# Performance work log

Measured on AMD Instinct MI355X. Metric: run time of the kernel, lower is better.

The kernel has to match this reference:

```python
import jax, jax.numpy as jnp
import numpy as np

B, T, H, HV, K, V = 8, 4096, 4, 8, 128, 128
SOFTPLUS_BETA = 1.0
SOFTPLUS_THRESHOLD = 20.0
USE_QK_L2NORM = True


def setup_inputs() -> dict:
    key = jax.random.key(0)
    ks = jax.random.split(key, 9)
    return {
        "A_log": jax.random.normal(ks[0], (HV,), jnp.float32) * 0.1,
        "a": jax.random.normal(ks[1], (B, T, HV), jnp.float32),
        "dt_bias": jax.random.normal(ks[2], (HV,), jnp.float32),
        "q": jax.random.normal(ks[3], (B, T, H, K), jnp.float32),
        "k": jax.random.normal(ks[4], (B, T, H, K), jnp.float32),
        "v": jax.random.normal(ks[5], (B, T, HV, V), jnp.float32),
        "b": jax.random.normal(ks[6], (B, T, HV), jnp.float32),
        "initial_state_source": jax.random.normal(ks[7], (B, HV, K, V), jnp.float32),
        "initial_state_indices": jax.random.randint(ks[8], (B,), 0, B, jnp.int32),
    }


def _softplus(x):
    # matches kernel: where(beta*x <= thr, log(1+exp(beta*x))/beta, x)
    bx = SOFTPLUS_BETA * x
    safe = jnp.minimum(bx, SOFTPLUS_THRESHOLD)  # avoid overflow in unused branch
    return jnp.where(bx <= SOFTPLUS_THRESHOLD, jnp.log1p(jnp.exp(safe)) / SOFTPLUS_BETA, x)


def _l2norm(x):
    # matches kernel: x / sqrt(sum(x^2) + 1e-6), over head dim
    return x / jnp.sqrt(jnp.sum(x * x, axis=-1, keepdims=True) + 1e-6)


def reference(A_log, a, dt_bias, q, k, v, b, initial_state_source, initial_state_indices):
    scale = K ** -0.5
    rep = HV // H  # GQA expansion: each q/k head serves `rep` value heads
    qe = jnp.repeat(q, rep, axis=2)  # [B,T,HV,K]
    ke = jnp.repeat(k, rep, axis=2)
    if USE_QK_L2NORM:
        qe = _l2norm(qe)
        ke = _l2norm(ke)
    qe = qe * scale

    g = -jnp.exp(A_log) * _softplus(a + dt_bias)  # [B,T,HV] log-decay
    beta = jax.nn.sigmoid(b)                      # [B,T,HV] write strength

    idx = initial_state_indices
    h0 = jnp.where((idx >= 0)[:, None, None, None],
                   initial_state_source[jnp.maximum(idx, 0)],
                   jnp.zeros((), jnp.float32))  # [B,HV,K,V]

    def step(h, xs):
        qt, kt, vt, gt, bt = xs  # [B,HV,K],[B,HV,K],[B,HV,V],[B,HV],[B,HV]
        h = h * jnp.exp(gt)[..., None, None]
        vt = (vt - jnp.einsum('nhkv,nhk->nhv', h, kt)) * bt[..., None]
        h = h + kt[..., None] * vt[..., None, :]
        ot = jnp.einsum('nhkv,nhk->nhv', h, qt)
        return h, ot

    xs = (qe.transpose(1, 0, 2, 3), ke.transpose(1, 0, 2, 3),
          v.transpose(1, 0, 2, 3), g.transpose(1, 0, 2), beta.transpose(1, 0, 2))
    _, o = jax.lax.scan(step, h0, xs)  # o: [T,B,HV,V]
    return o.transpose(1, 0, 2, 3)
```

## Files before the change

### kernel.cpp

```cpp
#include <hip/hip_runtime.h>
#include <math.h>

namespace {
constexpr int Bn = 8, Tn = 4096, Hn = 4, HVn = 8, Kn = 128, Vn = 128;
constexpr int CH = 8;
constexpr float SCALE = 0.088388347648318447f;
}

typedef float f2 __attribute__((ext_vector_type(2)));

template <int CTRL>
__device__ __forceinline__ float red_dpp(float x) {
  return x + __int_as_float(
      __builtin_amdgcn_mov_dpp(__float_as_int(x), CTRL, 0xF, 0xF, true));
}

__global__ __launch_bounds__(256) void gdn_prepass(
    const float* __restrict__ A_log, const float* __restrict__ a_in,
    const float* __restrict__ dt_bias, const float* __restrict__ q_in,
    const float* __restrict__ k_in, const float* __restrict__ b_in,
    float4* __restrict__ S)
{
  const int bt = blockIdx.x * 4 + (threadIdx.x >> 6);
  const int lane = threadIdx.x & 63;
  const int h  = lane >> 4;
  const int j0 = (lane & 15) * 8;

  const float* kp = k_in + ((long)bt * Hn + h) * Kn + j0;
  const float* qp = q_in + ((long)bt * Hn + h) * Kn + j0;
  const float4 ka = *(const float4*)kp;
  const float4 kb = *(const float4*)(kp + 4);
  const float4 qa = *(const float4*)qp;
  const float4 qb = *(const float4*)(qp + 4);

  float ks = ka.x*ka.x + ka.y*ka.y + ka.z*ka.z + ka.w*ka.w
           + kb.x*kb.x + kb.y*kb.y + kb.z*kb.z + kb.w*kb.w;
  float qs = qa.x*qa.x + qa.y*qa.y + qa.z*qa.z + qa.w*qa.w
           + qb.x*qb.x + qb.y*qb.y + qb.z*qb.z + qb.w*qb.w;
  ks = red_dpp<0xB1>(ks);  qs = red_dpp<0xB1>(qs);
  ks = red_dpp<0x4E>(ks);  qs = red_dpp<0x4E>(qs);
  ks = red_dpp<0x141>(ks); qs = red_dpp<0x141>(qs);
  ks = red_dpp<0x140>(ks); qs = red_dpp<0x140>(qs);
  const float rk = rsqrtf(ks + 1e-6f);
  const float rq = rsqrtf(qs + 1e-6f);

  const int src = (((lane & 7) >> 1) << 4);
  const float rkh = __shfl(rk, src);
  const float rqh = __shfl(rq, src);

  if (lane < 8) {
    const int hv = lane;
    const long sidx = (long)bt * HVn + hv;
    const float x  = a_in[sidx] + dt_bias[hv];
    const float sp = (x <= 20.0f) ? log1pf(expf(x)) : x;
    const float eg = expf(-expf(A_log[hv]) * sp);
    const float beta = 1.0f / (1.0f + expf(-b_in[sidx]));
    S[sidx] = make_float4(eg, beta * rkh, eg * rkh, rqh * SCALE);
  }
}

__device__ __forceinline__ void gll16(const float* g, float* l) {
  __builtin_amdgcn_global_load_lds(
      (const __attribute__((address_space(1))) void*)g,
      (__attribute__((address_space(3))) void*)l, 16, 0, 0);
}
__device__ __forceinline__ void gll4(const float* g, float* l) {
  __builtin_amdgcn_global_load_lds(
      (const __attribute__((address_space(1))) void*)g,
      (__attribute__((address_space(3))) void*)l, 4, 0, 0);
}

__device__ __forceinline__ float step2(f2 (&hs)[4],
    const float4 k0, const float4 k1, const float4 q0, const float4 q1,
    const float tv, const float4 ts)
{
  const f2 k0l = f2{k0.x,k0.y}, k0h = f2{k0.z,k0.w};
  const f2 k1l = f2{k1.x,k1.y}, k1h = f2{k1.z,k1.w};
  const f2 q0l = f2{q0.x,q0.y}, q0h = f2{q0.z,q0.w};
  const f2 q1l = f2{q1.x,q1.y}, q1h = f2{q1.z,q1.w};
  f2 d1 = f2{0.f,0.f}, d2 = f2{0.f,0.f}, d3 = f2{0.f,0.f};
  d1 = __builtin_elementwise_fma(hs[0], k0l, d1);
  d2 = __builtin_elementwise_fma(hs[0], q0l, d2);
  d3 = __builtin_elementwise_fma(k0l, q0l, d3);
  d1 = __builtin_elementwise_fma(hs[1], k0h, d1);
  d2 = __builtin_elementwise_fma(hs[1], q0h, d2);
  d3 = __builtin_elementwise_fma(k0h, q0h, d3);
  d1 = __builtin_elementwise_fma(hs[2], k1l, d1);
  d2 = __builtin_elementwise_fma(hs[2], q1l, d2);
  d3 = __builtin_elementwise_fma(k1l, q1l, d3);
  d1 = __builtin_elementwise_fma(hs[3], k1h, d1);
  d2 = __builtin_elementwise_fma(hs[3], q1h, d2);
  d3 = __builtin_elementwise_fma(k1h, q1h, d3);
  float s1 = d1.x + d1.y, s2 = d2.x + d2.y, s3 = d3.x + d3.y;
  s1 = red_dpp<0xB1>(s1);  s2 = red_dpp<0xB1>(s2);  s3 = red_dpp<0xB1>(s3);
  s1 = red_dpp<0x4E>(s1);  s2 = red_dpp<0x4E>(s2);  s3 = red_dpp<0x4E>(s3);
  s1 = red_dpp<0x141>(s1); s2 = red_dpp<0x141>(s2); s3 = red_dpp<0x141>(s3);
  s1 = red_dpp<0x140>(s1); s2 = red_dpp<0x140>(s2); s3 = red_dpp<0x140>(s3);
  const float c1 = ts.x;
  const float up = (tv - ts.z * s1) * ts.y;
  const float o  = fmaf(c1, s2, up * s3) * ts.w;
  const f2 c1v = f2{c1, c1}, upv = f2{up, up};
  hs[0] = __builtin_elementwise_fma(k0l, upv, hs[0] * c1v);
  hs[1] = __builtin_elementwise_fma(k0h, upv, hs[1] * c1v);
  hs[2] = __builtin_elementwise_fma(k1l, upv, hs[2] * c1v);
  hs[3] = __builtin_elementwise_fma(k1h, upv, hs[3] * c1v);
  return o;
}

__global__ __launch_bounds__(64, 2) void gdn_recurrent(
    const float* __restrict__ q_in, const float* __restrict__ k_in,
    const float* __restrict__ v_in, const float4* __restrict__ S,
    const float* __restrict__ h0_src, const int* __restrict__ h0_idx,
    float* __restrict__ out)
{
  const int blk  = blockIdx.x;
  const int g    = blk & 63;
  const int vblk = blk >> 6;
  const int b  = g >> 3;
  const int hv = g & 7;
  const int h  = hv >> 1;
  const int lane = threadIdx.x;
  const int kk  = lane & 15;
  const int vv  = lane >> 4;
  const int vg  = vblk * 4 + vv;
  const int kk4 = kk * 4;

  __shared__ __align__(16) float smK[2][CH][Kn];
  __shared__ __align__(16) float smQ[2][CH][Kn];
  __shared__ __align__(16) float smVS[2][64];

  const float* kst = k_in + (((long)b * Tn + (lane >> 5)) * Hn + h) * Kn + (lane & 31) * 4;
  const float* qst = q_in + (((long)b * Tn + (lane >> 5)) * Hn + h) * Kn + (lane & 31) * 4;
  const float* Sf  = (const float*)S;
  unsigned vsStride;
  const float* vsb;
  if (lane < 32) {
    vsStride = HVn * Vn;
    vsb = v_in + (((long)b * Tn + (lane >> 2)) * HVn + hv) * Vn + vblk * 4 + (lane & 3);
  } else {
    const int l2 = lane - 32;
    vsStride = HVn * 4;
    vsb = Sf + (((long)b * Tn + (l2 >> 2)) * HVn + hv) * 4 + (l2 & 3);
  }
  float* obp = out + (((long)b * Tn) * HVn + hv) * Vn + vg;

  f2 hs[4];
  {
    const int idx = h0_idx[b];
    if (idx >= 0) {
      const float* hp = h0_src + (((long)idx * HVn + hv) * Kn) * Vn + vg;
      hs[0] = f2{hp[(kk4+0)*Vn],    hp[(kk4+1)*Vn]};
      hs[1] = f2{hp[(kk4+2)*Vn],    hp[(kk4+3)*Vn]};
      hs[2] = f2{hp[(64+kk4+0)*Vn], hp[(64+kk4+1)*Vn]};
      hs[3] = f2{hp[(64+kk4+2)*Vn], hp[(64+kk4+3)*Vn]};
    } else {
      hs[0] = hs[1] = hs[2] = hs[3] = f2{0.f, 0.f};
    }
  }

#define STAGE(DB, TS0) {                                              \
    const unsigned kqo = (unsigned)(TS0) * (unsigned)(Hn * Kn);       \
    _Pragma("unroll")                                                 \
    for (int j_ = 0; j_ < 4; ++j_) {                                  \
      gll16(kst + kqo + j_ * 1024, &smK[DB][2*j_][0]);                \
      gll16(qst + kqo + j_ * 1024, &smQ[DB][2*j_][0]);                \
    }                                                                 \
    gll4(vsb + (unsigned)(TS0) * vsStride, &smVS[DB][0]); }

#define LDFRAG(P, DB, TL) {                                           \
    P##k0 = *(const float4*)&smK[DB][TL][kk4];                        \
    P##k1 = *(const float4*)&smK[DB][TL][64 + kk4];                   \
    P##q0 = *(const float4*)&smQ[DB][TL][kk4];                        \
    P##q1 = *(const float4*)&smQ[DB][TL][64 + kk4];                   \
    P##v  = smVS[DB][(TL) * 4 + vv];                                  \
    P##s  = *(const float4*)&smVS[DB][32 + (TL) * 4]; }

#define SB __builtin_amdgcn_sched_barrier(0)
#define STORE(T, O) { if (kk == 0) obp[(unsigned)((T) * (HVn * Vn))] = (O); }

  float4 Ak0, Ak1, Aq0, Aq1, As; float Av;
  float4 Bk0, Bk1, Bq0, Bq1, Bs; float Bv;

  STAGE(0, 0)
  asm volatile("s_waitcnt vmcnt(0)" ::: "memory");
  SB;
  LDFRAG(A, 0, 0)

#define BODY(BF, T0) {                                                          \
    const int ts0_ = ((T0) + CH < Tn) ? (T0) + CH : Tn - CH;                    \
    STAGE(BF ^ 1, ts0_)                                                         \
    SB;                                                                         \
    LDFRAG(B, BF, 1) SB; { const float o_ = step2(hs, Ak0,Ak1,Aq0,Aq1, Av, As); STORE((T0)+0, o_) } \
    LDFRAG(A, BF, 2) SB; { const float o_ = step2(hs, Bk0,Bk1,Bq0,Bq1, Bv, Bs); STORE((T0)+1, o_) } \
    LDFRAG(B, BF, 3) SB; { const float o_ = step2(hs, Ak0,Ak1,Aq0,Aq1, Av, As); STORE((T0)+2, o_) } \
    LDFRAG(A, BF, 4) SB; { const float o_ = step2(hs, Bk0,Bk1,Bq0,Bq1, Bv, Bs); STORE((T0)+3, o_) } \
    LDFRAG(B, BF, 5) SB; { const float o_ = step2(hs, Ak0,Ak1,Aq0,Aq1, Av, As); STORE((T0)+4, o_) } \
    LDFRAG(A, BF, 6) SB; { const float o_ = step2(hs, Bk0,Bk1,Bq0,Bq1, Bv, Bs); STORE((T0)+5, o_) } \
    LDFRAG(B, BF, 7) SB; { const float o_ = step2(hs, Ak0,Ak1,Aq0,Aq1, Av, As); STORE((T0)+6, o_) } \
    asm volatile("s_waitcnt vmcnt(7)" ::: "memory"); SB;                        \
    LDFRAG(A, BF ^ 1, 0) SB;                                                    \
    { const float o_ = step2(hs, Bk0,Bk1,Bq0,Bq1, Bv, Bs); STORE((T0)+7, o_) } }

  for (int t0 = 0; t0 < Tn; t0 += 2 * CH) {
    BODY(0, t0)
    BODY(1, t0 + CH)
  }
#undef BODY
#undef STAGE
#undef LDFRAG
#undef STORE
#undef SB
}

extern "C" void kernel_launch(void* const* d_in, const int* in_sizes, int n_in,
                              void* d_out, int out_size, void* d_ws, size_t ws_size,
                              hipStream_t stream) {
  const float* A_log = (const float*)d_in[0];
  const float* a_in  = (const float*)d_in[1];
  const float* dtb   = (const float*)d_in[2];
  const float* q_in  = (const float*)d_in[3];
  const float* k_in  = (const float*)d_in[4];
  const float* v_in  = (const float*)d_in[5];
  const float* b_in  = (const float*)d_in[6];
  const float* h0    = (const float*)d_in[7];
  const int*   idx   = (const int*)d_in[8];
  float* out = (float*)d_out;
  float4* S  = (float4*)d_ws;

  gdn_prepass<<<dim3(Bn * Tn / 4), dim3(256), 0, stream>>>(A_log, a_in, dtb,
                                                           q_in, k_in, b_in, S);
  gdn_recurrent<<<dim3(2048), dim3(64), 0, stream>>>(q_in, k_in, v_in, S,
                                                     h0, idx, out);
}
```

Measured before the change: 1.436 ms.

## Replace LDS double-buffer staging with direct register prefetch four steps ahead

The recurrent kernel no longer stages k/q/v/S through LDS with global_load_lds. Each lane now loads its own fragments straight into registers with inline-asm global loads, rotating four register sets so each timestep's loads are issued four steps ahead and gated by explicit vmcnt waits. Output stores are written in inline asm with an exec mask so only one lane per 16 stores, instead of a branch. The prepass also drops the cross-lane shuffle by having the lanes that own each head write S directly. This removes LDS traffic and LDS reads from the serial dependency chain, at the cost of more VGPRs and redundant global loads across lanes that depend on L1/L2 hits.

```diff
diff --git a/kernel.cpp b/kernel.cpp
--- a/kernel.cpp
+++ b/kernel.cpp
@@ -3,11 +3,11 @@
 
 namespace {
 constexpr int Bn = 8, Tn = 4096, Hn = 4, HVn = 8, Kn = 128, Vn = 128;
-constexpr int CH = 8;
 constexpr float SCALE = 0.088388347648318447f;
 }
 
 typedef float f2 __attribute__((ext_vector_type(2)));
+typedef float f4 __attribute__((ext_vector_type(4)));
 
 template <int CTRL>
 __device__ __forceinline__ float red_dpp(float x) {
@@ -44,35 +44,21 @@
   const float rk = rsqrtf(ks + 1e-6f);
   const float rq = rsqrtf(qs + 1e-6f);
 
-  const int src = (((lane & 7) >> 1) << 4);
-  const float rkh = __shfl(rk, src);
-  const float rqh = __shfl(rq, src);
-
-  if (lane < 8) {
-    const int hv = lane;
+  const int j = lane & 15;
+  if (j < 2) {
+    const int hv = 2 * h + j;
     const long sidx = (long)bt * HVn + hv;
     const float x  = a_in[sidx] + dt_bias[hv];
     const float sp = (x <= 20.0f) ? log1pf(expf(x)) : x;
     const float eg = expf(-expf(A_log[hv]) * sp);
     const float beta = 1.0f / (1.0f + expf(-b_in[sidx]));
-    S[sidx] = make_float4(eg, beta * rkh, eg * rkh, rqh * SCALE);
+    S[sidx] = make_float4(eg, beta * rk, eg * rk, rq * SCALE);
   }
 }
 
-__device__ __forceinline__ void gll16(const float* g, float* l) {
-  __builtin_amdgcn_global_load_lds(
-      (const __attribute__((address_space(1))) void*)g,
-      (__attribute__((address_space(3))) void*)l, 16, 0, 0);
-}
-__device__ __forceinline__ void gll4(const float* g, float* l) {
-  __builtin_amdgcn_global_load_lds(
-      (const __attribute__((address_space(1))) void*)g,
-      (__attribute__((address_space(3))) void*)l, 4, 0, 0);
-}
-
-__device__ __forceinline__ float step2(f2 (&hs)[4],
-    const float4 k0, const float4 k1, const float4 q0, const float4 q1,
-    const float tv, const float4 ts)
+__device__ __forceinline__ float core_step(f2 (&hs)[4],
+    const f4 k0, const f4 k1, const f4 q0, const f4 q1,
+    const float tv, const f4 ts)
 {
   const f2 k0l = f2{k0.x,k0.y}, k0h = f2{k0.z,k0.w};
   const f2 k1l = f2{k1.x,k1.y}, k1h = f2{k1.z,k1.w};
@@ -125,24 +111,17 @@
   const int vg  = vblk * 4 + vv;
   const int kk4 = kk * 4;
 
-  __shared__ __align__(16) float smK[2][CH][Kn];
-  __shared__ __align__(16) float smQ[2][CH][Kn];
-  __shared__ __align__(16) float smVS[2][64];
-
-  const float* kst = k_in + (((long)b * Tn + (lane >> 5)) * Hn + h) * Kn + (lane & 31) * 4;
-  const float* qst = q_in + (((long)b * Tn + (lane >> 5)) * Hn + h) * Kn + (lane & 31) * 4;
-  const float* Sf  = (const float*)S;
-  unsigned vsStride;
-  const float* vsb;
-  if (lane < 32) {
-    vsStride = HVn * Vn;
-    vsb = v_in + (((long)b * Tn + (lane >> 2)) * HVn + hv) * Vn + vblk * 4 + (lane & 3);
-  } else {
-    const int l2 = lane - 32;
-    vsStride = HVn * 4;
-    vsb = Sf + (((long)b * Tn + (l2 >> 2)) * HVn + hv) * 4 + (l2 & 3);
-  }
-  float* obp = out + (((long)b * Tn) * HVn + hv) * Vn + vg;
+  const float* kbp = k_in + ((long)b * Tn * Hn + h) * Kn;
+  const float* qbp = q_in + ((long)b * Tn * Hn + h) * Kn;
+  const float* vbp = v_in + ((long)b * Tn * HVn + hv) * Vn;
+  const f4*    sbp = ((const f4*)S) + (long)b * Tn * HVn + hv;
+  const float* obp = out + ((long)b * Tn * HVn + hv) * Vn;
+  const unsigned long long STMASK = 0x0001000100010001ULL;
+
+  unsigned voKQ = (unsigned)(kk * 16);
+  unsigned voV  = (unsigned)(vg * 4);
+  unsigned voS  = 0u;
+  unsigned voO  = (unsigned)(vg * 4);
 
   f2 hs[4];
   {
@@ -157,59 +136,73 @@
       hs[0] = hs[1] = hs[2] = hs[3] = f2{0.f, 0.f};
     }
   }
-
-#define STAGE(DB, TS0) {                                              \
-    const unsigned kqo = (unsigned)(TS0) * (unsigned)(Hn * Kn);       \
-    _Pragma("unroll")                                                 \
-    for (int j_ = 0; j_ < 4; ++j_) {                                  \
-      gll16(kst + kqo + j_ * 1024, &smK[DB][2*j_][0]);                \
-      gll16(qst + kqo + j_ * 1024, &smQ[DB][2*j_][0]);                \
-    }                                                                 \
-    gll4(vsb + (unsigned)(TS0) * vsStride, &smVS[DB][0]); }
-
-#define LDFRAG(P, DB, TL) {                                           \
-    P##k0 = *(const float4*)&smK[DB][TL][kk4];                        \
-    P##k1 = *(const float4*)&smK[DB][TL][64 + kk4];                   \
-    P##q0 = *(const float4*)&smQ[DB][TL][kk4];                        \
-    P##q1 = *(const float4*)&smQ[DB][TL][64 + kk4];                   \
-    P##v  = smVS[DB][(TL) * 4 + vv];                                  \
-    P##s  = *(const float4*)&smVS[DB][32 + (TL) * 4]; }
-
-#define SB __builtin_amdgcn_sched_barrier(0)
-#define STORE(T, O) { if (kk == 0) obp[(unsigned)((T) * (HVn * Vn))] = (O); }
-
-  float4 Ak0, Ak1, Aq0, Aq1, As; float Av;
-  float4 Bk0, Bk1, Bq0, Bq1, Bs; float Bv;
-
-  STAGE(0, 0)
   asm volatile("s_waitcnt vmcnt(0)" ::: "memory");
-  SB;
-  LDFRAG(A, 0, 0)
-
-#define BODY(BF, T0) {                                                          \
-    const int ts0_ = ((T0) + CH < Tn) ? (T0) + CH : Tn - CH;                    \
-    STAGE(BF ^ 1, ts0_)                                                         \
-    SB;                                                                         \
-    LDFRAG(B, BF, 1) SB; { const float o_ = step2(hs, Ak0,Ak1,Aq0,Aq1, Av, As); STORE((T0)+0, o_) } \
-    LDFRAG(A, BF, 2) SB; { const float o_ = step2(hs, Bk0,Bk1,Bq0,Bq1, Bv, Bs); STORE((T0)+1, o_) } \
-    LDFRAG(B, BF, 3) SB; { const float o_ = step2(hs, Ak0,Ak1,Aq0,Aq1, Av, As); STORE((T0)+2, o_) } \
-    LDFRAG(A, BF, 4) SB; { const float o_ = step2(hs, Bk0,Bk1,Bq0,Bq1, Bv, Bs); STORE((T0)+3, o_) } \
-    LDFRAG(B, BF, 5) SB; { const float o_ = step2(hs, Ak0,Ak1,Aq0,Aq1, Av, As); STORE((T0)+4, o_) } \
-    LDFRAG(A, BF, 6) SB; { const float o_ = step2(hs, Bk0,Bk1,Bq0,Bq1, Bv, Bs); STORE((T0)+5, o_) } \
-    LDFRAG(B, BF, 7) SB; { const float o_ = step2(hs, Ak0,Ak1,Aq0,Aq1, Av, As); STORE((T0)+6, o_) } \
-    asm volatile("s_waitcnt vmcnt(7)" ::: "memory"); SB;                        \
-    LDFRAG(A, BF ^ 1, 0) SB;                                                    \
-    { const float o_ = step2(hs, Bk0,Bk1,Bq0,Bq1, Bv, Bs); STORE((T0)+7, o_) } }
-
-  for (int t0 = 0; t0 < Tn; t0 += 2 * CH) {
-    BODY(0, t0)
-    BODY(1, t0 + CH)
+
+  f4 Ak0, Ak1, Aq0, Aq1, As; float Av;
+  f4 Bk0, Bk1, Bq0, Bq1, Bs; float Bv;
+  f4 Ck0, Ck1, Cq0, Cq1, Cs; float Cv;
+  f4 Dk0, Dk1, Dq0, Dq1, Ds; float Dv;
+
+#define GLK(P)                                                          \
+  asm volatile(                                                         \
+    "global_load_dwordx4 %0, %4, %5 offset:0\n\t"                       \
+    "global_load_dwordx4 %1, %4, %5 offset:256\n\t"                     \
+    "global_load_dwordx4 %2, %4, %6 offset:0\n\t"                       \
+    "global_load_dwordx4 %3, %4, %6 offset:256"                         \
+    : "=&v"(P##k0), "=&v"(P##k1), "=&v"(P##q0), "=&v"(P##q1)            \
+    : "v"(voKQ), "s"(kbp), "s"(qbp));
+
+#define GLVS(P)                                                         \
+  asm volatile(                                                         \
+    "global_load_dword %0, %2, %4\n\t"                                  \
+    "global_load_dwordx4 %1, %3, %5"                                    \
+    : "=&v"(P##v), "=&v"(P##s)                                          \
+    : "v"(voV), "v"(voS), "s"(vbp), "s"(sbp));
+
+#define ISSUE(P) GLK(P) GLVS(P)                                         \
+  voKQ += 2048u; voV += 4096u; voS += 128u;
+
+#define STORE(O)                                                        \
+  { unsigned long long sv_;                                             \
+    asm volatile("s_mov_b64 %0, exec\n\t"                               \
+                 "s_mov_b64 exec, %1\n\t"                               \
+                 "global_store_dword %2, %3, %4\n\t"                    \
+                 "s_mov_b64 exec, %0"                                   \
+                 : "=&s"(sv_)                                           \
+                 : "s"(STMASK), "v"(voO), "v"(O), "s"(obp)              \
+                 : "memory");                                           \
+    voO += 4096u; }
+
+#define WCNT_(N) asm volatile("s_waitcnt vmcnt(" #N ")" ::: "memory");  \
+  __builtin_amdgcn_sched_barrier(0);
+#define WCNT(N) WCNT_(N)
+
+#define STEP(P, WN) { WCNT(WN)                                          \
+  const float o_ = core_step(hs, P##k0, P##k1, P##q0, P##q1, P##v, P##s); \
+  ISSUE(P) STORE(o_) }
+
+#define STEPNL(P, WN) { WCNT(WN)                                        \
+  const float o_ = core_step(hs, P##k0, P##k1, P##q0, P##q1, P##v, P##s); \
+  STORE(o_) }
+
+  ISSUE(A) ISSUE(B) ISSUE(C) ISSUE(D)
+
+  STEP(A, 18) STEP(B, 19) STEP(C, 20) STEP(D, 21)
+
+  for (int it = 0; it < (Tn - 8) / 4; ++it) {
+    STEP(A, 22) STEP(B, 22) STEP(C, 22) STEP(D, 22)
   }
-#undef BODY
-#undef STAGE
-#undef LDFRAG
+
+  STEPNL(A, 22) STEPNL(B, 16) STEPNL(C, 10) STEPNL(D, 4)
+
+#undef GLK
+#undef GLVS
+#undef ISSUE
 #undef STORE
-#undef SB
+#undef WCNT_
+#undef WCNT
+#undef STEP
+#undef STEPNL
 }
 
 extern "C" void kernel_launch(void* const* d_in, const int* in_sizes, int n_in,
```

After: 1.781 ms. +24.0%, slower.
